# Performance work log

Measured on AMD Instinct MI355X. Metric: run time of the kernel, lower is better.

The kernel has to match this reference:

```python
import jax, jax.numpy as jnp
import numpy as np
from fractions import Fraction
from math import factorial, sqrt

# ---------- e3nn-convention real Wigner 3j, unit Frobenius norm ----------
def _su2_cg(j1, m1, j2, m2, j3, m3):
    if m3 != m1 + m2:
        return 0.0
    f = lambda n: factorial(int(n))
    vmin = int(max(-j1 + j2 + m3, -j1 + m1, 0))
    vmax = int(min(j2 + j3 + m1, j3 - j1 + j2, j3 + m3))
    C = ((2.0 * j3 + 1.0) * Fraction(
        f(j3 + j1 - j2) * f(j3 - j1 + j2) * f(j1 + j2 - j3) * f(j3 + m3) * f(j3 - m3),
        f(j1 + j2 + j3 + 1) * f(j1 - m1) * f(j1 + m1) * f(j2 - m2) * f(j2 + m2))) ** 0.5
    S = Fraction(0)
    for v in range(vmin, vmax + 1):
        S += (-1) ** int(v + j2 + m2) * Fraction(
            f(j2 + j3 + m1 - v) * f(j1 - m1 + v),
            f(v) * f(j3 - j1 + j2 - v) * f(j3 + m3 - v) * f(v + j1 - j2 - m3))
    return float(C) * float(S)

def _q(l):  # real->complex spherical-harmonic change of basis (e3nn convention)
    q = np.zeros((2 * l + 1, 2 * l + 1), dtype=np.complex128)
    for m in range(-l, 0):
        q[l + m, l + abs(m)] = 1 / 2 ** 0.5
        q[l + m, l - abs(m)] = -1j / 2 ** 0.5
    q[l, l] = 1
    for m in range(1, l + 1):
        q[l + m, l + abs(m)] = (-1) ** m / 2 ** 0.5
        q[l + m, l - abs(m)] = 1j * (-1) ** m / 2 ** 0.5
    return (-1j) ** l * q

def wigner_3j(l1, l2, l3):
    cg = np.zeros((2 * l1 + 1, 2 * l2 + 1, 2 * l3 + 1))
    for m1 in range(-l1, l1 + 1):
        for m2 in range(-l2, l2 + 1):
            if abs(m1 + m2) <= l3:
                cg[l1 + m1, l2 + m2, l3 + m1 + m2] = _su2_cg(l1, m1, l2, m2, l3, m1 + m2)
    C = np.einsum('ij,kl,mn,ikn->jlm', _q(l1), _q(l2), np.conj(_q(l3).T), cg.astype(np.complex128))
    C = np.real(C)
    return (C / np.linalg.norm(C)).astype(np.float32)

# ---------- TensorProduct config: 32x0e+32x1o+32x2e (x) same -> same, all uvw paths ----------
MUL = 32
LS = (0, 1, 2)
OFF = (0, MUL * 1, MUL * 1 + MUL * 3)  # block offsets in the flat 288-dim layout
DIM = MUL * (1 + 3 + 5)                # 288
INS = [(0, 0, 0), (1, 1, 0), (2, 2, 0),
       (0, 1, 1), (1, 0, 1), (1, 2, 1), (2, 1, 1),
       (0, 2, 2), (1, 1, 2), (2, 0, 2), (2, 2, 2)]
_counts = {io: sum(1 for i in INS if i[2] == io) for io in set(i[2] for i in INS)}
# 'component' normalization: scale unit-norm w3j by sqrt(2*l_out+1); uvw mode: alpha=sqrt(path_weight/(n_paths_to_out*mul1*mul2))
ALPHA = [sqrt((2 * LS[io] + 1) / (_counts[io] * MUL * MUL)) for (_, _, io) in INS]
W3J = {(LS[i1], LS[i2], LS[io]): wigner_3j(LS[i1], LS[i2], LS[io]) for (i1, i2, io) in INS}


def setup_inputs() -> dict:
    key = jax.random.key(0)
    k1, k2, k3 = jax.random.split(key, 3)
    B = 2048
    return {
        'x1': jax.random.normal(k1, (B, DIM), dtype=jnp.float32),
        'x2': jax.random.normal(k2, (B, DIM), dtype=jnp.float32),
        'ws': jax.random.normal(k3, (len(INS), MUL, MUL, MUL), dtype=jnp.float32),
    }


def reference(x1, x2, ws):
    B = x1.shape[0]
    out = jnp.zeros((B, DIM), dtype=x1.dtype)
    for p, (i1, i2, io) in enumerate(INS):
        l1, l2, lo = LS[i1], LS[i2], LS[io]
        s1 = x1[:, OFF[i1]:OFF[i1] + MUL * (2 * l1 + 1)].reshape(B, MUL, 2 * l1 + 1)
        s2 = x2[:, OFF[i2]:OFF[i2] + MUL * (2 * l2 + 1)].reshape(B, MUL, 2 * l2 + 1)
        C = jnp.asarray(W3J[(l1, l2, lo)], dtype=x1.dtype)
        # z u v w: batch, mul_in1, mul_in2, mul_out ; i j k: 2l+1 components
        r = jnp.einsum('uvw,ijk,zui,zvj->zwk', ws[p], C, s1, s2)
        out = out.at[:, OFF[io]:OFF[io] + MUL * (2 * lo + 1)].add(ALPHA[p] * r.reshape(B, -1))
    return out
```

## Files before the change

kernel.cpp:

```cpp
#include <hip/hip_runtime.h>
#include <hip/hip_bf16.h>
#include <cmath>
#include <complex>
#include <algorithm>


typedef std::complex<double> cd;

static double factd(int n) { double r = 1; for (int i = 2; i <= n; ++i) r *= i; return r; }

static double su2_cg(int j1, int m1, int j2, int m2, int j3, int m3) {
    if (m3 != m1 + m2) return 0.0;
    int vmin = std::max(std::max(-j1 + j2 + m3, -j1 + m1), 0);
    int vmax = std::min(std::min(j2 + j3 + m1, j3 - j1 + j2), j3 + m3);
    double C = std::sqrt((2.0 * j3 + 1.0) *
        (factd(j3 + j1 - j2) * factd(j3 - j1 + j2) * factd(j1 + j2 - j3) *
         factd(j3 + m3) * factd(j3 - m3)) /
        (factd(j1 + j2 + j3 + 1) * factd(j1 - m1) * factd(j1 + m1) *
         factd(j2 - m2) * factd(j2 + m2)));
    double S = 0.0;
    for (int v = vmin; v <= vmax; ++v) {
        double sgn = ((v + j2 + m2) & 1) ? -1.0 : 1.0;
        S += sgn * (factd(j2 + j3 + m1 - v) * factd(j1 - m1 + v)) /
             (factd(v) * factd(j3 - j1 + j2 - v) * factd(j3 + m3 - v) *
              factd(v + j1 - j2 - m3));
    }
    return C * S;
}

static void qmat(int l, cd* q) {
    int n = 2 * l + 1;
    for (int i = 0; i < n * n; ++i) q[i] = cd(0, 0);
    const double s = 1.0 / std::sqrt(2.0);
    for (int m = -l; m < 0; ++m) {
        q[(l + m) * n + (l - m)] = cd(s, 0);
        q[(l + m) * n + (l + m)] = cd(0, -s);
    }
    q[l * n + l] = cd(1, 0);
    for (int m = 1; m <= l; ++m) {
        double sg = (m & 1) ? -1.0 : 1.0;
        q[(l + m) * n + (l + m)] = cd(sg * s, 0);
        q[(l + m) * n + (l - m)] = cd(0, sg * s);
    }
    cd ph(1, 0);
    for (int t = 0; t < l; ++t) ph *= cd(0, -1);
    for (int i = 0; i < n * n; ++i) q[i] *= ph;
}

static void wigner3j_dense(int l1, int l2, int l3, double* outp) {
    int n1 = 2 * l1 + 1, n2 = 2 * l2 + 1, n3 = 2 * l3 + 1;
    double cg[125];
    for (int i = 0; i < n1 * n2 * n3; ++i) cg[i] = 0.0;
    for (int m1 = -l1; m1 <= l1; ++m1)
        for (int m2 = -l2; m2 <= l2; ++m2) {
            int m3 = m1 + m2;
            if (std::abs(m3) <= l3)
                cg[((l1 + m1) * n2 + (l2 + m2)) * n3 + (l3 + m3)] =
                    su2_cg(l1, m1, l2, m2, l3, m3);
        }
    cd q1[25], q2[25], q3[25];
    qmat(l1, q1); qmat(l2, q2); qmat(l3, q3);
    double norm2 = 0.0;
    for (int j = 0; j < n1; ++j)
        for (int l = 0; l < n2; ++l)
            for (int m = 0; m < n3; ++m) {
                cd sum(0, 0);
                for (int i = 0; i < n1; ++i)
                    for (int k = 0; k < n2; ++k)
                        for (int n = 0; n < n3; ++n) {
                            double g = cg[(i * n2 + k) * n3 + n];
                            if (g != 0.0)
                                sum += q1[i * n1 + j] * q2[k * n2 + l] *
                                       std::conj(q3[n * n3 + m]) * g;
                        }
                outp[(j * n2 + l) * n3 + m] = sum.real();
                norm2 += sum.real() * sum.real();
            }
    double inv = 1.0 / std::sqrt(norm2);
    for (int t = 0; t < n1 * n2 * n3; ++t) outp[t] *= inv;
}


struct E3 { unsigned char i, j, k; };

constexpr E3 PAT_P0[1]  = {{0,0,0}};
constexpr E3 PAT_P1[3]  = {{0,0,0},{1,1,0},{2,2,0}};
constexpr E3 PAT_P2[5]  = {{0,0,0},{1,1,0},{2,2,0},{3,3,0},{4,4,0}};
constexpr E3 PAT_P3[3]  = {{0,0,0},{0,1,1},{0,2,2}};
constexpr E3 PAT_P4[3]  = {{0,0,0},{1,0,1},{2,0,2}};
constexpr E3 PAT_P5[11] = {{1,2,1},{1,3,2},{1,1,0},{2,2,2},{0,2,0},{2,3,1},
                           {0,1,1},{2,4,2},{0,0,2},{2,0,0},{0,4,0}};
constexpr E3 PAT_P6[11] = {{2,1,1},{2,2,2},{2,0,0},{3,1,2},{1,1,0},{3,2,1},
                           {1,0,1},{4,2,2},{0,0,2},{4,0,0},{0,2,0}};
constexpr E3 PAT_P7[5]  = {{0,0,0},{0,1,1},{0,2,2},{0,3,3},{0,4,4}};
constexpr E3 PAT_P8[11] = {{1,1,2},{1,2,3},{1,0,1},{2,1,3},{0,1,1},{2,2,2},
                           {0,0,2},{2,2,4},{0,0,4},{2,0,0},{0,2,0}};
constexpr E3 PAT_P9[5]  = {{0,0,0},{1,0,1},{2,0,2},{3,0,3},{4,0,4}};
constexpr E3 PAT_P10[25]= {{2,2,2},{2,3,3},{2,1,1},{2,4,4},{2,0,0},{3,2,3},
                           {1,2,1},{3,3,2},{1,1,2},{3,3,4},{1,1,4},{3,1,0},
                           {1,3,0},{3,4,3},{1,0,3},{3,0,1},{1,4,1},{4,2,4},
                           {0,2,0},{4,3,3},{0,1,3},{4,1,1},{0,3,1},{4,4,2},
                           {0,0,2}};

constexpr int OFF_P[11] = {0, 1, 4, 9, 12, 15, 26, 37, 42, 53, 58};

struct W3JArg { float c[83]; };

static W3JArg build_w3j_sparse() {
    struct PD { const E3* pat; int ne; int l1, l2, lo; double alpha; };
    const double a0 = std::sqrt(1.0/3072.0), a1 = std::sqrt(3.0/4096.0),
                 a2 = std::sqrt(5.0/4096.0);
    const PD pd[11] = {
        {PAT_P0, 1, 0,0,0, a0}, {PAT_P1, 3, 1,1,0, a0}, {PAT_P2, 5, 2,2,0, a0},
        {PAT_P3, 3, 0,1,1, a1}, {PAT_P4, 3, 1,0,1, a1}, {PAT_P5,11, 1,2,1, a1},
        {PAT_P6,11, 2,1,1, a1}, {PAT_P7, 5, 0,2,2, a2}, {PAT_P8,11, 1,1,2, a2},
        {PAT_P9, 5, 2,0,2, a2}, {PAT_P10,25,2,2,2, a2}
    };
    W3JArg arg;
    for (int p = 0; p < 11; ++p) {
        double dense[125];
        wigner3j_dense(pd[p].l1, pd[p].l2, pd[p].lo, dense);
        int n2 = 2*pd[p].l2+1, n3 = 2*pd[p].lo+1;
        for (int e = 0; e < pd[p].ne; ++e) {
            const E3& t = pd[p].pat[e];
            arg.c[OFF_P[p] + e] =
                (float)(dense[(t.i * n2 + t.j) * n3 + t.k] * pd[p].alpha);
        }
    }
    return arg;
}


typedef __attribute__((ext_vector_type(8))) short short8;
typedef __attribute__((ext_vector_type(4))) float f32x4;

__device__ __forceinline__ unsigned short f2bf_bits(float f) {
    __hip_bfloat16 h = __float2bfloat16(f);
    unsigned short u; __builtin_memcpy(&u, &h, 2); return u;
}

template<int NE, int A1, int A2, int D3, int SBASE, int SSTR>
__device__ __forceinline__ void do_path(const E3 (&pat)[NE],
                                        const float* __restrict__ cs,
                                        const float* a, const float* b0,
                                        const float* b1,
                                        unsigned* __restrict__ dst) {
    float t0[D3], t1[D3];
    #pragma unroll
    for (int k = 0; k < D3; ++k) { t0[k] = 0.0f; t1[k] = 0.0f; }
    #pragma unroll
    for (int e = 0; e < NE; ++e) {
        const float c = cs[e];
        const float av = a[A1 + pat[e].i];
        const int k = pat[e].k;
        t0[k] = fmaf(c, av * b0[A2 + pat[e].j], t0[k]);
        t1[k] = fmaf(c, av * b1[A2 + pat[e].j], t1[k]);
    }
    #pragma unroll
    for (int k = 0; k < D3; ++k) {
        float2 f2; f2.x = t0[k]; f2.y = t1[k];
        __hip_bfloat162 pk = __float22bfloat162_rn(f2);
        unsigned u; __builtin_memcpy(&u, &pk, 4);
        dst[(SBASE + k * SSTR) * 256] = u;
    }
}

__device__ __forceinline__ void build_all(const float* __restrict__ cs,
                                          const float* a, const float* b0,
                                          const float* b1,
                                          unsigned* __restrict__ dst) {
    do_path< 1,0,0,1, 0,1>(PAT_P0,  cs +  0, a, b0, b1, dst);
    do_path< 3,1,1,1, 1,1>(PAT_P1,  cs +  1, a, b0, b1, dst);
    do_path< 5,4,4,1, 2,1>(PAT_P2,  cs +  4, a, b0, b1, dst);
    do_path< 3,0,1,3, 3,4>(PAT_P3,  cs +  9, a, b0, b1, dst);
    do_path< 3,1,0,3, 4,4>(PAT_P4,  cs + 12, a, b0, b1, dst);
    do_path<11,1,4,3, 5,4>(PAT_P5,  cs + 15, a, b0, b1, dst);
    do_path<11,4,1,3, 6,4>(PAT_P6,  cs + 26, a, b0, b1, dst);
    do_path< 5,0,4,5,15,4>(PAT_P7,  cs + 37, a, b0, b1, dst);
    do_path<11,1,1,5,16,4>(PAT_P8,  cs + 42, a, b0, b1, dst);
    do_path< 5,4,0,5,17,4>(PAT_P9,  cs + 53, a, b0, b1, dst);
    do_path<25,4,4,5,18,4>(PAT_P10, cs + 58, a, b0, b1, dst);
}

template<bool USE_WST>
__device__ __forceinline__ short8 load_bfrag(const float* __restrict__ ws,
                                             const unsigned short* __restrict__ wsT,
                                             int p, int u, int w, int vbase) {
    if constexpr (USE_WST) {
        return *(const short8*)(wsT + (((size_t)(p*32+u)*32 + w)*32 + vbase));
    } else {
        short8 r;
        #pragma unroll
        for (int j = 0; j < 8; ++j) {
            float f = ws[((size_t)(p*32+u)*32 + (vbase+j))*32 + w];
            r[j] = (short)f2bf_bits(f);
        }
        return r;
    }
}

__global__ void ws_prep(const float* __restrict__ ws,
                        unsigned short* __restrict__ wsT,
                        float* __restrict__ out) {
    __shared__ float tile[32][33];
    const int pu = blockIdx.x, tid = threadIdx.x;
    const float4 f = ((const float4*)(ws + (size_t)pu * 1024))[tid];
    const int v = tid >> 3, w0 = (tid & 7) * 4;
    tile[v][w0+0] = f.x; tile[v][w0+1] = f.y; tile[v][w0+2] = f.z; tile[v][w0+3] = f.w;

    float4 z4; z4.x = z4.y = z4.z = z4.w = 0.0f;
    for (int i = blockIdx.x * 256 + tid; i < 147456; i += 352 * 256)
        ((float4*)out)[i] = z4;

    __syncthreads();
    const int w = tid >> 3, vB = (tid & 7) * 4;
    ushort4 o;
    o.x = f2bf_bits(tile[vB+0][w]); o.y = f2bf_bits(tile[vB+1][w]);
    o.z = f2bf_bits(tile[vB+2][w]); o.w = f2bf_bits(tile[vB+3][w]);
    *(ushort4*)(wsT + (size_t)pu * 1024 + tid * 4) = o;
}

template<bool USE_WST>
__launch_bounds__(256, 3)
__global__ void tp_mfma(const float* __restrict__ x1, const float* __restrict__ x2,
                        const float* __restrict__ ws, const unsigned short* __restrict__ wsT,
                        float* __restrict__ out, W3JArg w3j) {
    __shared__ unsigned shT[35 * 256];
    __shared__ float x1s[16 * 288];

    const int tid = threadIdx.x;
    const int l = tid & 63, wv = tid >> 6, kh = wv & 1, nt = wv >> 1;
    const int z0 = (blockIdx.x >> 2) * 16, u0 = (blockIdx.x & 3) * 8;

    for (int i = tid; i < 16 * 72; i += 256)
        ((float4*)x1s)[i] = ((const float4*)(x1 + (size_t)z0 * 288))[i];

    const int tz = tid >> 4, vp = tid & 15, v0 = vp * 2;

    float b0[9], b1[9];
    {
        const float* xr = x2 + (size_t)(z0 + tz) * 288;
        b0[0] = xr[v0]; b1[0] = xr[v0 + 1];
        #pragma unroll
        for (int j = 0; j < 3; ++j) { b0[1+j] = xr[32 + v0*3 + j]; b1[1+j] = xr[32 + (v0+1)*3 + j]; }
        #pragma unroll
        for (int j = 0; j < 5; ++j) { b0[4+j] = xr[128 + v0*5 + j]; b1[4+j] = xr[128 + (v0+1)*5 + j]; }
    }

    unsigned* dstT = shT + tz * 16 + (vp & 3) + ((((vp >> 2) + (tz >> 1)) & 3) << 2);
    const unsigned* tbase = shT + (l & 15) * 16 +
                            ((((l >> 4) + ((l & 15) >> 1)) & 3) << 2);

    const int w  = (l & 15) + nt * 16;
    const int vb = (l >> 4) * 8;

    f32x4 acc[5];
    #pragma unroll
    for (int i = 0; i < 5; ++i) acc[i] = (f32x4)(0.0f);

    __syncthreads();

    for (int ui = 0; ui < 8; ++ui) {
        const int u = u0 + ui;

        short8 bf[7];
        if (kh == 0) {
            #pragma unroll
            for (int p = 0; p < 7; ++p) bf[p] = load_bfrag<USE_WST>(ws, wsT, p, u, w, vb);
        } else {
            #pragma unroll
            for (int p = 0; p < 4; ++p) bf[p] = load_bfrag<USE_WST>(ws, wsT, 7 + p, u, w, vb);
        }

        float a[9];
        {
            const float* xr = x1s + tz * 288;
            a[0] = xr[u];
            #pragma unroll
            for (int i = 0; i < 3; ++i) a[1+i] = xr[32 + u*3 + i];
            #pragma unroll
            for (int i = 0; i < 5; ++i) a[4+i] = xr[128 + u*5 + i];
        }

        __syncthreads();
        build_all(w3j.c, a, b0, b1, dstT);
        __syncthreads();

        if (kh == 0) {
            #pragma unroll
            for (int m = 0; m < 3; ++m) {
                short8 af = *(const short8*)(tbase + m * 256);
                acc[0] = __builtin_amdgcn_mfma_f32_16x16x32_bf16(af, bf[m], acc[0], 0, 0, 0);
            }
            #pragma unroll
            for (int g = 0; g < 3; ++g)
                #pragma unroll
                for (int m = 0; m < 4; ++m) {
                    short8 af = *(const short8*)(tbase + (3 + g*4 + m) * 256);
                    acc[1+g] = __builtin_amdgcn_mfma_f32_16x16x32_bf16(af, bf[3+m], acc[1+g], 0, 0, 0);
                }
        } else {
            #pragma unroll
            for (int g = 0; g < 5; ++g)
                #pragma unroll
                for (int m = 0; m < 4; ++m) {
                    short8 af = *(const short8*)(tbase + (15 + g*4 + m) * 256);
                    acc[g] = __builtin_amdgcn_mfma_f32_16x16x32_bf16(af, bf[m], acc[g], 0, 0, 0);
                }
        }
    }

    const int zr = z0 + ((l >> 4) << 2);
    if (kh == 0) {
        #pragma unroll
        for (int r = 0; r < 4; ++r)
            atomicAdd(&out[(size_t)(zr + r) * 288 + w], acc[0][r]);
        #pragma unroll
        for (int k = 0; k < 3; ++k)
            #pragma unroll
            for (int r = 0; r < 4; ++r)
                atomicAdd(&out[(size_t)(zr + r) * 288 + 32 + w*3 + k], acc[1+k][r]);
    } else {
        #pragma unroll
        for (int k = 0; k < 5; ++k)
            #pragma unroll
            for (int r = 0; r < 4; ++r)
                atomicAdd(&out[(size_t)(zr + r) * 288 + 128 + w*5 + k], acc[k][r]);
    }
}


extern "C" void kernel_launch(void* const* d_in, const int* in_sizes, int n_in,
                              void* d_out, int out_size, void* d_ws, size_t ws_size,
                              hipStream_t stream) {
    const float* x1 = (const float*)d_in[0];
    const float* x2 = (const float*)d_in[1];
    const float* ws = (const float*)d_in[2];
    float* out = (float*)d_out;

    static const W3JArg arg = build_w3j_sparse();

    const int B = in_sizes[0] / 288;
    const int grid = (B / 16) * 4;

    const size_t wst_bytes = (size_t)11 * 32 * 32 * 32 * 2;
    unsigned short* wsT = (unsigned short*)d_ws;
    if (ws_size >= wst_bytes) {
        ws_prep<<<dim3(11 * 32), dim3(256), 0, stream>>>(ws, wsT, out);
        tp_mfma<true><<<dim3(grid), dim3(256), 0, stream>>>(x1, x2, ws, wsT, out, arg);
    } else {
        hipMemsetAsync(out, 0, (size_t)out_size * sizeof(float), stream);
        tp_mfma<false><<<dim3(grid), dim3(256), 0, stream>>>(x1, x2, ws, wsT, out, arg);
    }
}
```

Measured before the change: 106.5 us.

## Double-buffer shared tensor build and prefetch weights, drop ws_prep pre-pass

Removes the separate weight transpose/bf16 conversion kernel and instead loads fp32 weights directly in registers per wave, converting them in-loop, with the next u's weights and x1 row prefetched while the current step computes. The shared-memory product tensor is double-buffered so only one barrier per iteration is needed, and the wave work split is changed so each wave covers both 16-wide w tiles for a subset of paths (6 accumulators). It also precomputes c*a products in the path builder and vectorizes x2 loads. This trades an extra kernel launch and a transposed-weight buffer for strided fp32 global loads, doubled LDS, and higher register pressure (occupancy bound lowered to 2).

```diff
diff --git a/kernel.cpp b/kernel.cpp
--- a/kernel.cpp
+++ b/kernel.cpp
@@ -134,9 +134,10 @@
 typedef __attribute__((ext_vector_type(8))) short short8;
 typedef __attribute__((ext_vector_type(4))) float f32x4;
 
-__device__ __forceinline__ unsigned short f2bf_bits(float f) {
-    __hip_bfloat16 h = __float2bfloat16(f);
-    unsigned short u; __builtin_memcpy(&u, &h, 2); return u;
+__device__ __forceinline__ unsigned pack2(float lo, float hi) {
+    float2 f2; f2.x = lo; f2.y = hi;
+    __hip_bfloat162 pk = __float22bfloat162_rn(f2);
+    unsigned u; __builtin_memcpy(&u, &pk, 4); return u;
 }
 
 template<int NE, int A1, int A2, int D3, int SBASE, int SSTR>
@@ -145,24 +146,21 @@
                                         const float* a, const float* b0,
                                         const float* b1,
                                         unsigned* __restrict__ dst) {
+    float ca[NE];
+    #pragma unroll
+    for (int e = 0; e < NE; ++e) ca[e] = cs[e] * a[A1 + pat[e].i];
     float t0[D3], t1[D3];
     #pragma unroll
     for (int k = 0; k < D3; ++k) { t0[k] = 0.0f; t1[k] = 0.0f; }
     #pragma unroll
     for (int e = 0; e < NE; ++e) {
-        const float c = cs[e];
-        const float av = a[A1 + pat[e].i];
         const int k = pat[e].k;
-        t0[k] = fmaf(c, av * b0[A2 + pat[e].j], t0[k]);
-        t1[k] = fmaf(c, av * b1[A2 + pat[e].j], t1[k]);
-    }
-    #pragma unroll
-    for (int k = 0; k < D3; ++k) {
-        float2 f2; f2.x = t0[k]; f2.y = t1[k];
-        __hip_bfloat162 pk = __float22bfloat162_rn(f2);
-        unsigned u; __builtin_memcpy(&u, &pk, 4);
-        dst[(SBASE + k * SSTR) * 256] = u;
-    }
+        t0[k] = fmaf(ca[e], b0[A2 + pat[e].j], t0[k]);
+        t1[k] = fmaf(ca[e], b1[A2 + pat[e].j], t1[k]);
+    }
+    #pragma unroll
+    for (int k = 0; k < D3; ++k)
+        dst[(SBASE + k * SSTR) * 256] = pack2(t0[k], t1[k]);
 }
 
 __device__ __forceinline__ void build_all(const float* __restrict__ cs,
@@ -182,150 +180,185 @@
     do_path<25,4,4,5,18,4>(PAT_P10, cs + 58, a, b0, b1, dst);
 }
 
-template<bool USE_WST>
-__device__ __forceinline__ short8 load_bfrag(const float* __restrict__ ws,
-                                             const unsigned short* __restrict__ wsT,
-                                             int p, int u, int w, int vbase) {
-    if constexpr (USE_WST) {
-        return *(const short8*)(wsT + (((size_t)(p*32+u)*32 + w)*32 + vbase));
-    } else {
-        short8 r;
-        #pragma unroll
-        for (int j = 0; j < 8; ++j) {
-            float f = ws[((size_t)(p*32+u)*32 + (vbase+j))*32 + w];
-            r[j] = (short)f2bf_bits(f);
-        }
-        return r;
-    }
-}
-
-__global__ void ws_prep(const float* __restrict__ ws,
-                        unsigned short* __restrict__ wsT,
-                        float* __restrict__ out) {
-    __shared__ float tile[32][33];
-    const int pu = blockIdx.x, tid = threadIdx.x;
-    const float4 f = ((const float4*)(ws + (size_t)pu * 1024))[tid];
-    const int v = tid >> 3, w0 = (tid & 7) * 4;
-    tile[v][w0+0] = f.x; tile[v][w0+1] = f.y; tile[v][w0+2] = f.z; tile[v][w0+3] = f.w;
-
-    float4 z4; z4.x = z4.y = z4.z = z4.w = 0.0f;
-    for (int i = blockIdx.x * 256 + tid; i < 147456; i += 352 * 256)
-        ((float4*)out)[i] = z4;
-
-    __syncthreads();
-    const int w = tid >> 3, vB = (tid & 7) * 4;
-    ushort4 o;
-    o.x = f2bf_bits(tile[vB+0][w]); o.y = f2bf_bits(tile[vB+1][w]);
-    o.z = f2bf_bits(tile[vB+2][w]); o.w = f2bf_bits(tile[vB+3][w]);
-    *(ushort4*)(wsT + (size_t)pu * 1024 + tid * 4) = o;
-}
-
-template<bool USE_WST>
-__launch_bounds__(256, 3)
-__global__ void tp_mfma(const float* __restrict__ x1, const float* __restrict__ x2,
-                        const float* __restrict__ ws, const unsigned short* __restrict__ wsT,
+__device__ __forceinline__ void load_a(const float* __restrict__ x1r, int u,
+                                       float* a) {
+    a[0] = x1r[u];
+    #pragma unroll
+    for (int i = 0; i < 3; ++i) a[1 + i] = x1r[32 + u * 3 + i];
+    #pragma unroll
+    for (int i = 0; i < 5; ++i) a[4 + i] = x1r[128 + u * 5 + i];
+}
+
+__device__ __forceinline__ void load_b(const float* __restrict__ ws,
+                                       int pbase, int u, int l,
+                                       float (&bfr)[8][8]) {
+    const int w_lo = l & 15, vb = (l >> 4) * 8;
+    #pragma unroll
+    for (int f = 0; f < 8; ++f) {
+        const int p = pbase + (f >> 1);
+        const int w = w_lo + (f & 1) * 16;
+        const float* base = ws + (((size_t)(p * 32 + u) * 32 + vb) * 32 + w);
+        #pragma unroll
+        for (int j = 0; j < 8; ++j) bfr[f][j] = base[j * 32];
+    }
+}
+
+__device__ __forceinline__ void cvt_frags(const float (&bfr)[8][8],
+                                          short8 (&bf)[8]) {
+    #pragma unroll
+    for (int f = 0; f < 8; ++f) {
+        unsigned tmp[4];
+        #pragma unroll
+        for (int j2 = 0; j2 < 4; ++j2)
+            tmp[j2] = pack2(bfr[f][2 * j2], bfr[f][2 * j2 + 1]);
+        __builtin_memcpy(&bf[f], tmp, 16);
+    }
+}
+
+
+#define SHT_WORDS (35 * 256)
+
+__launch_bounds__(256, 2)
+__global__ void tp_mfma(const float* __restrict__ x1,
+                        const float* __restrict__ x2,
+                        const float* __restrict__ ws,
                         float* __restrict__ out, W3JArg w3j) {
-    __shared__ unsigned shT[35 * 256];
-    __shared__ float x1s[16 * 288];
+    __shared__ unsigned shT[2 * SHT_WORDS];
 
     const int tid = threadIdx.x;
-    const int l = tid & 63, wv = tid >> 6, kh = wv & 1, nt = wv >> 1;
+    const int l = tid & 63, wv = tid >> 6;
     const int z0 = (blockIdx.x >> 2) * 16, u0 = (blockIdx.x & 3) * 8;
-
-    for (int i = tid; i < 16 * 72; i += 256)
-        ((float4*)x1s)[i] = ((const float4*)(x1 + (size_t)z0 * 288))[i];
-
     const int tz = tid >> 4, vp = tid & 15, v0 = vp * 2;
 
     float b0[9], b1[9];
     {
         const float* xr = x2 + (size_t)(z0 + tz) * 288;
-        b0[0] = xr[v0]; b1[0] = xr[v0 + 1];
-        #pragma unroll
-        for (int j = 0; j < 3; ++j) { b0[1+j] = xr[32 + v0*3 + j]; b1[1+j] = xr[32 + (v0+1)*3 + j]; }
-        #pragma unroll
-        for (int j = 0; j < 5; ++j) { b0[4+j] = xr[128 + v0*5 + j]; b1[4+j] = xr[128 + (v0+1)*5 + j]; }
-    }
-
-    unsigned* dstT = shT + tz * 16 + (vp & 3) + ((((vp >> 2) + (tz >> 1)) & 3) << 2);
-    const unsigned* tbase = shT + (l & 15) * 16 +
-                            ((((l >> 4) + ((l & 15) >> 1)) & 3) << 2);
-
-    const int w  = (l & 15) + nt * 16;
-    const int vb = (l >> 4) * 8;
-
-    f32x4 acc[5];
-    #pragma unroll
-    for (int i = 0; i < 5; ++i) acc[i] = (f32x4)(0.0f);
-
-    __syncthreads();
-
+        float2 s0 = *(const float2*)(xr + v0);
+        b0[0] = s0.x; b1[0] = s0.y;
+        const float* p1 = xr + 32 + v0 * 3;
+        float2 q0 = *(const float2*)(p1 + 0);
+        float2 q1 = *(const float2*)(p1 + 2);
+        float2 q2 = *(const float2*)(p1 + 4);
+        b0[1] = q0.x; b0[2] = q0.y; b0[3] = q1.x;
+        b1[1] = q1.y; b1[2] = q2.x; b1[3] = q2.y;
+        const float* p2 = xr + 128 + v0 * 5;
+        #pragma unroll
+        for (int h = 0; h < 5; ++h) {
+            float2 r = *(const float2*)(p2 + 2 * h);
+            float vlo = r.x, vhi = r.y;
+            if (2 * h < 5) b0[4 + 2 * h] = vlo; else b1[4 + 2 * h - 5] = vlo;
+            if (2 * h + 1 < 5) b0[5 + 2 * h] = vhi; else b1[4 + 2 * h - 4] = vhi;
+        }
+    }
+
+    const float* x1r = x1 + (size_t)(z0 + tz) * 288;
+    const int pbase = (wv == 0) ? 0 : (wv == 1) ? 3 : 7;
+
+    float a[2][9];
+    load_a(x1r, u0, a[0]);
+
+    float bfr[8][8];
+    load_b(ws, pbase, u0, l, bfr);
+
+    unsigned* dstbase = shT + tz * 16 + (vp & 3) + ((((vp >> 2) + (tz >> 1)) & 3) << 2);
+    const unsigned* tb0 = shT + (l & 15) * 16 + ((((l >> 4) + ((l & 15) >> 1)) & 3) << 2);
+
+    f32x4 acc[6];
+    #pragma unroll
+    for (int i = 0; i < 6; ++i) acc[i] = (f32x4)(0.0f);
+
+    short8 bf[8];
+
+    #pragma unroll 2
     for (int ui = 0; ui < 8; ++ui) {
-        const int u = u0 + ui;
-
-        short8 bf[7];
-        if (kh == 0) {
-            #pragma unroll
-            for (int p = 0; p < 7; ++p) bf[p] = load_bfrag<USE_WST>(ws, wsT, p, u, w, vb);
-        } else {
-            #pragma unroll
-            for (int p = 0; p < 4; ++p) bf[p] = load_bfrag<USE_WST>(ws, wsT, 7 + p, u, w, vb);
-        }
-
-        float a[9];
-        {
-            const float* xr = x1s + tz * 288;
-            a[0] = xr[u];
-            #pragma unroll
-            for (int i = 0; i < 3; ++i) a[1+i] = xr[32 + u*3 + i];
-            #pragma unroll
-            for (int i = 0; i < 5; ++i) a[4+i] = xr[128 + u*5 + i];
-        }
+        const int cur = ui & 1;
+        if (ui < 7) load_a(x1r, u0 + ui + 1, a[cur ^ 1]);
+
+        build_all(w3j.c, a[cur], b0, b1, dstbase + cur * SHT_WORDS);
+        cvt_frags(bfr, bf);
 
         __syncthreads();
-        build_all(w3j.c, a, b0, b1, dstT);
-        __syncthreads();
-
-        if (kh == 0) {
+
+        if (ui < 7) load_b(ws, pbase, u0 + ui + 1, l, bfr);
+
+        const unsigned* tb = tb0 + cur * SHT_WORDS;
+        if (wv == 0) {
             #pragma unroll
             for (int m = 0; m < 3; ++m) {
-                short8 af = *(const short8*)(tbase + m * 256);
-                acc[0] = __builtin_amdgcn_mfma_f32_16x16x32_bf16(af, bf[m], acc[0], 0, 0, 0);
-            }
-            #pragma unroll
-            for (int g = 0; g < 3; ++g)
+                short8 af = *(const short8*)(tb + m * 256);
+                acc[0] = __builtin_amdgcn_mfma_f32_16x16x32_bf16(af, bf[2*m+0], acc[0], 0, 0, 0);
+                acc[1] = __builtin_amdgcn_mfma_f32_16x16x32_bf16(af, bf[2*m+1], acc[1], 0, 0, 0);
+            }
+        } else if (wv == 1) {
+            #pragma unroll
+            for (int kk = 0; kk < 3; ++kk)
                 #pragma unroll
                 for (int m = 0; m < 4; ++m) {
-                    short8 af = *(const short8*)(tbase + (3 + g*4 + m) * 256);
-                    acc[1+g] = __builtin_amdgcn_mfma_f32_16x16x32_bf16(af, bf[3+m], acc[1+g], 0, 0, 0);
+                    short8 af = *(const short8*)(tb + (3 + kk * 4 + m) * 256);
+                    acc[2*kk+0] = __builtin_amdgcn_mfma_f32_16x16x32_bf16(af, bf[2*m+0], acc[2*kk+0], 0, 0, 0);
+                    acc[2*kk+1] = __builtin_amdgcn_mfma_f32_16x16x32_bf16(af, bf[2*m+1], acc[2*kk+1], 0, 0, 0);
+                }
+        } else if (wv == 2) {
+            #pragma unroll
+            for (int kk = 0; kk < 2; ++kk)
+                #pragma unroll
+                for (int m = 0; m < 4; ++m) {
+                    short8 af = *(const short8*)(tb + (15 + kk * 4 + m) * 256);
+                    acc[2*kk+0] = __builtin_amdgcn_mfma_f32_16x16x32_bf16(af, bf[2*m+0], acc[2*kk+0], 0, 0, 0);
+                    acc[2*kk+1] = __builtin_amdgcn_mfma_f32_16x16x32_bf16(af, bf[2*m+1], acc[2*kk+1], 0, 0, 0);
                 }
         } else {
             #pragma unroll
-            for (int g = 0; g < 5; ++g)
+            for (int kk = 2; kk < 5; ++kk)
                 #pragma unroll
                 for (int m = 0; m < 4; ++m) {
-                    short8 af = *(const short8*)(tbase + (15 + g*4 + m) * 256);
-                    acc[g] = __builtin_amdgcn_mfma_f32_16x16x32_bf16(af, bf[m], acc[g], 0, 0, 0);
+                    short8 af = *(const short8*)(tb + (15 + kk * 4 + m) * 256);
+                    acc[2*(kk-2)+0] = __builtin_amdgcn_mfma_f32_16x16x32_bf16(af, bf[2*m+0], acc[2*(kk-2)+0], 0, 0, 0);
+                    acc[2*(kk-2)+1] = __builtin_amdgcn_mfma_f32_16x16x32_bf16(af, bf[2*m+1], acc[2*(kk-2)+1], 0, 0, 0);
                 }
         }
     }
 
     const int zr = z0 + ((l >> 4) << 2);
-    if (kh == 0) {
-        #pragma unroll
-        for (int r = 0; r < 4; ++r)
-            atomicAdd(&out[(size_t)(zr + r) * 288 + w], acc[0][r]);
-        #pragma unroll
-        for (int k = 0; k < 3; ++k)
+    const int wl = l & 15;
+    if (wv == 0) {
+        #pragma unroll
+        for (int nt = 0; nt < 2; ++nt) {
+            const int w = wl + nt * 16;
             #pragma unroll
             for (int r = 0; r < 4; ++r)
-                atomicAdd(&out[(size_t)(zr + r) * 288 + 32 + w*3 + k], acc[1+k][r]);
+                atomicAdd(&out[(size_t)(zr + r) * 288 + w], acc[nt][r]);
+        }
+    } else if (wv == 1) {
+        #pragma unroll
+        for (int kk = 0; kk < 3; ++kk)
+            #pragma unroll
+            for (int nt = 0; nt < 2; ++nt) {
+                const int w = wl + nt * 16;
+                #pragma unroll
+                for (int r = 0; r < 4; ++r)
+                    atomicAdd(&out[(size_t)(zr + r) * 288 + 32 + w * 3 + kk], acc[2*kk+nt][r]);
+            }
+    } else if (wv == 2) {
+        #pragma unroll
+        for (int kk = 0; kk < 2; ++kk)
+            #pragma unroll
+            for (int nt = 0; nt < 2; ++nt) {
+                const int w = wl + nt * 16;
+                #pragma unroll
+                for (int r = 0; r < 4; ++r)
+                    atomicAdd(&out[(size_t)(zr + r) * 288 + 128 + w * 5 + kk], acc[2*kk+nt][r]);
+            }
     } else {
         #pragma unroll
-        for (int k = 0; k < 5; ++k)
-            #pragma unroll
-            for (int r = 0; r < 4; ++r)
-                atomicAdd(&out[(size_t)(zr + r) * 288 + 128 + w*5 + k], acc[k][r]);
+        for (int kk = 2; kk < 5; ++kk)
+            #pragma unroll
+            for (int nt = 0; nt < 2; ++nt) {
+                const int w = wl + nt * 16;
+                #pragma unroll
+                for (int r = 0; r < 4; ++r)
+                    atomicAdd(&out[(size_t)(zr + r) * 288 + 128 + w * 5 + kk], acc[2*(kk-2)+nt][r]);
+            }
     }
 }
 
@@ -343,13 +376,6 @@
     const int B = in_sizes[0] / 288;
     const int grid = (B / 16) * 4;
 
-    const size_t wst_bytes = (size_t)11 * 32 * 32 * 32 * 2;
-    unsigned short* wsT = (unsigned short*)d_ws;
-    if (ws_size >= wst_bytes) {
-        ws_prep<<<dim3(11 * 32), dim3(256), 0, stream>>>(ws, wsT, out);
-        tp_mfma<true><<<dim3(grid), dim3(256), 0, stream>>>(x1, x2, ws, wsT, out, arg);
-    } else {
-        hipMemsetAsync(out, 0, (size_t)out_size * sizeof(float), stream);
-        tp_mfma<false><<<dim3(grid), dim3(256), 0, stream>>>(x1, x2, ws, wsT, out, arg);
-    }
-}
+    hipMemsetAsync(out, 0, (size_t)out_size * sizeof(float), stream);
+    tp_mfma<<<dim3(grid), dim3(256), 0, stream>>>(x1, x2, ws, out, arg);
+}
```

Result: slower. 117.3 us (+10.1%).

## Split u range finer across blocks, drop x1 smem staging, prefetch x1 rows

Applied to the files above, without the earlier changes.

Each block now handles 4 u values instead of 8, doubling the grid to 8*(B/16) blocks and reordering the block index so z varies fastest. The x1 shared-memory tile is removed, and the per-u x1 values are read directly from global memory with a double-buffered register prefetch of the next u. The kernel also vectorises the x2 loads into float2, precomputes c*a products in the sparse W3J builder, and raises the launch-bounds occupancy hint to 4. The cost is twice as many atomic adds to the output and more redundant x2 and W3J build work per z row.

```diff
diff --git a/kernel.cpp b/kernel.cpp
--- a/kernel.cpp
+++ b/kernel.cpp
@@ -139,30 +139,33 @@
     unsigned short u; __builtin_memcpy(&u, &h, 2); return u;
 }
 
+__device__ __forceinline__ unsigned pack2(float lo, float hi) {
+    float2 f2; f2.x = lo; f2.y = hi;
+    __hip_bfloat162 pk = __float22bfloat162_rn(f2);
+    unsigned u; __builtin_memcpy(&u, &pk, 4); return u;
+}
+
 template<int NE, int A1, int A2, int D3, int SBASE, int SSTR>
 __device__ __forceinline__ void do_path(const E3 (&pat)[NE],
                                         const float* __restrict__ cs,
                                         const float* a, const float* b0,
                                         const float* b1,
                                         unsigned* __restrict__ dst) {
+    float ca[NE];
+    #pragma unroll
+    for (int e = 0; e < NE; ++e) ca[e] = cs[e] * a[A1 + pat[e].i];
     float t0[D3], t1[D3];
     #pragma unroll
     for (int k = 0; k < D3; ++k) { t0[k] = 0.0f; t1[k] = 0.0f; }
     #pragma unroll
     for (int e = 0; e < NE; ++e) {
-        const float c = cs[e];
-        const float av = a[A1 + pat[e].i];
         const int k = pat[e].k;
-        t0[k] = fmaf(c, av * b0[A2 + pat[e].j], t0[k]);
-        t1[k] = fmaf(c, av * b1[A2 + pat[e].j], t1[k]);
-    }
-    #pragma unroll
-    for (int k = 0; k < D3; ++k) {
-        float2 f2; f2.x = t0[k]; f2.y = t1[k];
-        __hip_bfloat162 pk = __float22bfloat162_rn(f2);
-        unsigned u; __builtin_memcpy(&u, &pk, 4);
-        dst[(SBASE + k * SSTR) * 256] = u;
-    }
+        t0[k] = fmaf(ca[e], b0[A2 + pat[e].j], t0[k]);
+        t1[k] = fmaf(ca[e], b1[A2 + pat[e].j], t1[k]);
+    }
+    #pragma unroll
+    for (int k = 0; k < D3; ++k)
+        dst[(SBASE + k * SSTR) * 256] = pack2(t0[k], t1[k]);
 }
 
 __device__ __forceinline__ void build_all(const float* __restrict__ cs,
@@ -182,6 +185,15 @@
     do_path<25,4,4,5,18,4>(PAT_P10, cs + 58, a, b0, b1, dst);
 }
 
+__device__ __forceinline__ void load_a(const float* __restrict__ x1r, int u,
+                                       float* a) {
+    a[0] = x1r[u];
+    #pragma unroll
+    for (int i = 0; i < 3; ++i) a[1 + i] = x1r[32 + u * 3 + i];
+    #pragma unroll
+    for (int i = 0; i < 5; ++i) a[4 + i] = x1r[128 + u * 5 + i];
+}
+
 template<bool USE_WST>
 __device__ __forceinline__ short8 load_bfrag(const float* __restrict__ ws,
                                              const unsigned short* __restrict__ wsT,
@@ -220,32 +232,42 @@
     *(ushort4*)(wsT + (size_t)pu * 1024 + tid * 4) = o;
 }
 
-template<bool USE_WST>
-__launch_bounds__(256, 3)
-__global__ void tp_mfma(const float* __restrict__ x1, const float* __restrict__ x2,
-                        const float* __restrict__ ws, const unsigned short* __restrict__ wsT,
+
+__launch_bounds__(256, 4)
+__global__ void tp_mfma(const float* __restrict__ x1,
+                        const float* __restrict__ x2,
+                        const float* __restrict__ ws,
+                        const unsigned short* __restrict__ wsT,
                         float* __restrict__ out, W3JArg w3j) {
     __shared__ unsigned shT[35 * 256];
-    __shared__ float x1s[16 * 288];
 
     const int tid = threadIdx.x;
     const int l = tid & 63, wv = tid >> 6, kh = wv & 1, nt = wv >> 1;
-    const int z0 = (blockIdx.x >> 2) * 16, u0 = (blockIdx.x & 3) * 8;
-
-    for (int i = tid; i < 16 * 72; i += 256)
-        ((float4*)x1s)[i] = ((const float4*)(x1 + (size_t)z0 * 288))[i];
-
+    const int z0 = (blockIdx.x & 127) * 16;
+    const int u0 = (blockIdx.x >> 7) * 4;
     const int tz = tid >> 4, vp = tid & 15, v0 = vp * 2;
 
     float b0[9], b1[9];
     {
         const float* xr = x2 + (size_t)(z0 + tz) * 288;
-        b0[0] = xr[v0]; b1[0] = xr[v0 + 1];
-        #pragma unroll
-        for (int j = 0; j < 3; ++j) { b0[1+j] = xr[32 + v0*3 + j]; b1[1+j] = xr[32 + (v0+1)*3 + j]; }
-        #pragma unroll
-        for (int j = 0; j < 5; ++j) { b0[4+j] = xr[128 + v0*5 + j]; b1[4+j] = xr[128 + (v0+1)*5 + j]; }
-    }
+        float2 s0 = *(const float2*)(xr + v0);
+        b0[0] = s0.x; b1[0] = s0.y;
+        const float* p1 = xr + 32 + v0 * 3;
+        float2 q0 = *(const float2*)(p1 + 0);
+        float2 q1 = *(const float2*)(p1 + 2);
+        float2 q2 = *(const float2*)(p1 + 4);
+        b0[1] = q0.x; b0[2] = q0.y; b0[3] = q1.x;
+        b1[1] = q1.y; b1[2] = q2.x; b1[3] = q2.y;
+        const float* p2 = xr + 128 + v0 * 5;
+        #pragma unroll
+        for (int h = 0; h < 5; ++h) {
+            float2 r = *(const float2*)(p2 + 2 * h);
+            if (2 * h < 5) b0[4 + 2 * h] = r.x; else b1[4 + 2 * h - 5] = r.x;
+            if (2 * h + 1 < 5) b0[5 + 2 * h] = r.y; else b1[4 + 2 * h - 4] = r.y;
+        }
+    }
+
+    const float* x1r = x1 + (size_t)(z0 + tz) * 288;
 
     unsigned* dstT = shT + tz * 16 + (vp & 3) + ((((vp >> 2) + (tz >> 1)) & 3) << 2);
     const unsigned* tbase = shT + (l & 15) * 16 +
@@ -258,32 +280,26 @@
     #pragma unroll
     for (int i = 0; i < 5; ++i) acc[i] = (f32x4)(0.0f);
 
-    __syncthreads();
-
-    for (int ui = 0; ui < 8; ++ui) {
+    float a[2][9];
+    load_a(x1r, u0, a[0]);
+
+    for (int ui = 0; ui < 4; ++ui) {
         const int u = u0 + ui;
+        const int cur = ui & 1;
 
         short8 bf[7];
         if (kh == 0) {
             #pragma unroll
-            for (int p = 0; p < 7; ++p) bf[p] = load_bfrag<USE_WST>(ws, wsT, p, u, w, vb);
+            for (int p = 0; p < 7; ++p) bf[p] = load_bfrag<true>(ws, wsT, p, u, w, vb);
         } else {
             #pragma unroll
-            for (int p = 0; p < 4; ++p) bf[p] = load_bfrag<USE_WST>(ws, wsT, 7 + p, u, w, vb);
-        }
-
-        float a[9];
-        {
-            const float* xr = x1s + tz * 288;
-            a[0] = xr[u];
-            #pragma unroll
-            for (int i = 0; i < 3; ++i) a[1+i] = xr[32 + u*3 + i];
-            #pragma unroll
-            for (int i = 0; i < 5; ++i) a[4+i] = xr[128 + u*5 + i];
-        }
+            for (int p = 0; p < 4; ++p) bf[p] = load_bfrag<true>(ws, wsT, 7 + p, u, w, vb);
+        }
+
+        if (ui < 3) load_a(x1r, u + 1, a[cur ^ 1]);
 
         __syncthreads();
-        build_all(w3j.c, a, b0, b1, dstT);
+        build_all(w3j.c, a[cur], b0, b1, dstT);
         __syncthreads();
 
         if (kh == 0) {
@@ -329,6 +345,107 @@
     }
 }
 
+__launch_bounds__(256, 4)
+__global__ void tp_mfma_nowst(const float* __restrict__ x1,
+                              const float* __restrict__ x2,
+                              const float* __restrict__ ws,
+                              float* __restrict__ out, W3JArg w3j) {
+    __shared__ unsigned shT[35 * 256];
+    const int tid = threadIdx.x;
+    const int l = tid & 63, wv = tid >> 6, kh = wv & 1, nt = wv >> 1;
+    const int z0 = (blockIdx.x & 127) * 16;
+    const int u0 = (blockIdx.x >> 7) * 4;
+    const int tz = tid >> 4, vp = tid & 15, v0 = vp * 2;
+
+    float b0[9], b1[9];
+    {
+        const float* xr = x2 + (size_t)(z0 + tz) * 288;
+        float2 s0 = *(const float2*)(xr + v0);
+        b0[0] = s0.x; b1[0] = s0.y;
+        const float* p1 = xr + 32 + v0 * 3;
+        float2 q0 = *(const float2*)(p1 + 0);
+        float2 q1 = *(const float2*)(p1 + 2);
+        float2 q2 = *(const float2*)(p1 + 4);
+        b0[1] = q0.x; b0[2] = q0.y; b0[3] = q1.x;
+        b1[1] = q1.y; b1[2] = q2.x; b1[3] = q2.y;
+        const float* p2 = xr + 128 + v0 * 5;
+        #pragma unroll
+        for (int h = 0; h < 5; ++h) {
+            float2 r = *(const float2*)(p2 + 2 * h);
+            if (2 * h < 5) b0[4 + 2 * h] = r.x; else b1[4 + 2 * h - 5] = r.x;
+            if (2 * h + 1 < 5) b0[5 + 2 * h] = r.y; else b1[4 + 2 * h - 4] = r.y;
+        }
+    }
+    const float* x1r = x1 + (size_t)(z0 + tz) * 288;
+    unsigned* dstT = shT + tz * 16 + (vp & 3) + ((((vp >> 2) + (tz >> 1)) & 3) << 2);
+    const unsigned* tbase = shT + (l & 15) * 16 +
+                            ((((l >> 4) + ((l & 15) >> 1)) & 3) << 2);
+    const int w  = (l & 15) + nt * 16;
+    const int vb = (l >> 4) * 8;
+
+    f32x4 acc[5];
+    #pragma unroll
+    for (int i = 0; i < 5; ++i) acc[i] = (f32x4)(0.0f);
+    float a[2][9];
+    load_a(x1r, u0, a[0]);
+
+    for (int ui = 0; ui < 4; ++ui) {
+        const int u = u0 + ui;
+        const int cur = ui & 1;
+        short8 bf[7];
+        if (kh == 0) {
+            #pragma unroll
+            for (int p = 0; p < 7; ++p) bf[p] = load_bfrag<false>(ws, nullptr, p, u, w, vb);
+        } else {
+            #pragma unroll
+            for (int p = 0; p < 4; ++p) bf[p] = load_bfrag<false>(ws, nullptr, 7 + p, u, w, vb);
+        }
+        if (ui < 3) load_a(x1r, u + 1, a[cur ^ 1]);
+        __syncthreads();
+        build_all(w3j.c, a[cur], b0, b1, dstT);
+        __syncthreads();
+        if (kh == 0) {
+            #pragma unroll
+            for (int m = 0; m < 3; ++m) {
+                short8 af = *(const short8*)(tbase + m * 256);
+                acc[0] = __builtin_amdgcn_mfma_f32_16x16x32_bf16(af, bf[m], acc[0], 0, 0, 0);
+            }
+            #pragma unroll
+            for (int g = 0; g < 3; ++g)
+                #pragma unroll
+                for (int m = 0; m < 4; ++m) {
+                    short8 af = *(const short8*)(tbase + (3 + g*4 + m) * 256);
+                    acc[1+g] = __builtin_amdgcn_mfma_f32_16x16x32_bf16(af, bf[3+m], acc[1+g], 0, 0, 0);
+                }
+        } else {
+            #pragma unroll
+            for (int g = 0; g < 5; ++g)
+                #pragma unroll
+                for (int m = 0; m < 4; ++m) {
+                    short8 af = *(const short8*)(tbase + (15 + g*4 + m) * 256);
+                    acc[g] = __builtin_amdgcn_mfma_f32_16x16x32_bf16(af, bf[m], acc[g], 0, 0, 0);
+                }
+        }
+    }
+    const int zr = z0 + ((l >> 4) << 2);
+    if (kh == 0) {
+        #pragma unroll
+        for (int r = 0; r < 4; ++r)
+            atomicAdd(&out[(size_t)(zr + r) * 288 + w], acc[0][r]);
+        #pragma unroll
+        for (int k = 0; k < 3; ++k)
+            #pragma unroll
+            for (int r = 0; r < 4; ++r)
+                atomicAdd(&out[(size_t)(zr + r) * 288 + 32 + w*3 + k], acc[1+k][r]);
+    } else {
+        #pragma unroll
+        for (int k = 0; k < 5; ++k)
+            #pragma unroll
+            for (int r = 0; r < 4; ++r)
+                atomicAdd(&out[(size_t)(zr + r) * 288 + 128 + w*5 + k], acc[k][r]);
+    }
+}
+
 
 extern "C" void kernel_launch(void* const* d_in, const int* in_sizes, int n_in,
                               void* d_out, int out_size, void* d_ws, size_t ws_size,
@@ -341,15 +458,15 @@
     static const W3JArg arg = build_w3j_sparse();
 
     const int B = in_sizes[0] / 288;
-    const int grid = (B / 16) * 4;
+    const int grid = 8 * (B / 16);
 
     const size_t wst_bytes = (size_t)11 * 32 * 32 * 32 * 2;
     unsigned short* wsT = (unsigned short*)d_ws;
     if (ws_size >= wst_bytes) {
         ws_prep<<<dim3(11 * 32), dim3(256), 0, stream>>>(ws, wsT, out);
-        tp_mfma<true><<<dim3(grid), dim3(256), 0, stream>>>(x1, x2, ws, wsT, out, arg);
+        tp_mfma<<<dim3(grid), dim3(256), 0, stream>>>(x1, x2, ws, wsT, out, arg);
     } else {
         hipMemsetAsync(out, 0, (size_t)out_size * sizeof(float), stream);
-        tp_mfma<false><<<dim3(grid), dim3(256), 0, stream>>>(x1, x2, ws, wsT, out, arg);
-    }
-}
+        tp_mfma_nowst<<<dim3(grid), dim3(256), 0, stream>>>(x1, x2, ws, out, arg);
+    }
+}
```

Result: slower. 124.3 us (+16.7%).
